# Performance work log

Measured on AMD Instinct MI355X. Metric: run time of the kernel, lower is better.

The kernel has to match this reference:

```python
import jax, jax.numpy as jnp
import numpy as np

N = 100000
E = 1600000
IN_FEATS = 128
HID = 128


def _xavier(key, shape):
    fan_in, fan_out = shape[0], shape[1]
    limit = float(np.sqrt(6.0 / (fan_in + fan_out)))
    return jax.random.uniform(key, shape, jnp.float32, -limit, limit)


def setup_inputs() -> dict:
    key = jax.random.key(0)
    ks = jax.random.split(key, 10)
    x = jax.random.normal(ks[0], (N, IN_FEATS), jnp.float32)
    edge_index = jax.random.randint(ks[1], (2, E), 0, N, jnp.int64)
    inp = {"x": x, "edge_index": edge_index}
    # GCNConv weights (stored as [in, out] so h = x @ W)
    inp["W1"] = _xavier(ks[2], (IN_FEATS, HID)); inp["b1"] = jnp.zeros((HID,), jnp.float32)
    inp["W2"] = _xavier(ks[3], (HID, HID));      inp["b2"] = jnp.zeros((HID,), jnp.float32)
    inp["W3"] = _xavier(ks[4], (HID, HID));      inp["b3"] = jnp.zeros((HID,), jnp.float32)
    # position head: Linear(HID,HID) -> ReLU -> Linear(HID,2)
    inp["Wp1"] = _xavier(ks[5], (HID, HID)); inp["bp1"] = jnp.zeros((HID,), jnp.float32)
    inp["Wp2"] = _xavier(ks[6], (HID, 2));   inp["bp2"] = jnp.zeros((2,), jnp.float32)
    # time head: Linear(HID,HID//2) -> ReLU -> Linear(HID//2,1)
    inp["Wt1"] = _xavier(ks[7], (HID, HID // 2)); inp["bt1"] = jnp.zeros((HID // 2,), jnp.float32)
    inp["Wt2"] = _xavier(ks[8], (HID // 2, 1));   inp["bt2"] = jnp.zeros((1,), jnp.float32)
    return inp


def _gcn_conv(x, src, dst, norm, W, b):
    # PyG GCNConv: out = D^{-1/2} (A + I) D^{-1/2} (x W) + b
    h = x @ W                                  # [N, out]
    msg = h[src] * norm[:, None]               # gather over edges (+ self-loops)
    agg = jax.ops.segment_sum(msg, dst, num_segments=N)  # scatter-add to dst
    return agg + b


def reference(x, edge_index, W1, b1, W2, b2, W3, b3, Wp1, bp1, Wp2, bp2, Wt1, bt1, Wt2, bt2):
    src, dst = edge_index[0], edge_index[1]
    # add self-loops once (shared across the 3 conv layers)
    loop = jnp.arange(N, dtype=edge_index.dtype)
    src_a = jnp.concatenate([src, loop])
    dst_a = jnp.concatenate([dst, loop])
    # symmetric normalization: deg computed on dst (in-degree incl. self-loop)
    deg = jax.ops.segment_sum(jnp.ones_like(dst_a, dtype=x.dtype), dst_a, num_segments=N)
    dinv = jnp.where(deg > 0, jax.lax.rsqrt(deg), 0.0)
    norm = dinv[src_a] * dinv[dst_a]           # [E + N]

    h = jax.nn.relu(_gcn_conv(x, src_a, dst_a, norm, W1, b1))
    h = jax.nn.relu(_gcn_conv(h, src_a, dst_a, norm, W2, b2))
    h = jax.nn.relu(_gcn_conv(h, src_a, dst_a, norm, W3, b3))

    pos = jax.nn.relu(h @ Wp1 + bp1) @ Wp2 + bp2     # [N, 2]
    time = jax.nn.relu(h @ Wt1 + bt1) @ Wt2 + bt2    # [N, 1]
    return jnp.concatenate([pos, time], axis=1)      # [N, 3]
```

## Files before the change

kernel.cpp:

```cpp
#include <hip/hip_runtime.h>

typedef __bf16 bf16x8 __attribute__((ext_vector_type(8)));
typedef unsigned short u16x8 __attribute__((ext_vector_type(8)));
typedef float f32x4 __attribute__((ext_vector_type(4)));

union BU {
    u16x8 u;
    bf16x8 b;
};

static __device__ __forceinline__ float b2f(unsigned short u) {
    return __uint_as_float(((unsigned)u) << 16);
}
static __device__ __forceinline__ unsigned short f2b(float f) {
    unsigned u = __float_as_uint(f);
    unsigned r = (u + 0x7FFF + ((u >> 16) & 1)) >> 16;
    return (unsigned short)r;
}

__global__ __launch_bounds__(256) void wsplit_kernel(
    const float* __restrict__ W1, const float* __restrict__ W2, const float* __restrict__ W3,
    const float* __restrict__ Wp1, const float* __restrict__ Wt1,
    unsigned short* __restrict__ W1hi, unsigned short* __restrict__ W1lo,
    unsigned short* __restrict__ W2hi, unsigned short* __restrict__ W2lo,
    unsigned short* __restrict__ W3hi, unsigned short* __restrict__ W3lo,
    unsigned short* __restrict__ Wchi, unsigned short* __restrict__ Wclo,
    const float* __restrict__ bp1, const float* __restrict__ bt1, float* __restrict__ bcat) {
    int b = blockIdx.x;
    int tid = threadIdx.x;
    if (b < 288) {
        const float* W;
        unsigned short *Whi, *Wlo;
        int lb, ncshift, total;
        if (b < 64)       { W = W1;  Whi = W1hi; Wlo = W1lo; lb = b;       ncshift = 7; total = 16384; }
        else if (b < 128) { W = W2;  Whi = W2hi; Wlo = W2lo; lb = b - 64;  ncshift = 7; total = 16384; }
        else if (b < 192) { W = W3;  Whi = W3hi; Wlo = W3lo; lb = b - 128; ncshift = 7; total = 16384; }
        else if (b < 256) { W = Wp1; Whi = Wchi; Wlo = Wclo; lb = b - 192; ncshift = 7; total = 16384; }
        else              { W = Wt1; Whi = Wchi + 128 * 128; Wlo = Wclo + 128 * 128; lb = b - 256; ncshift = 6; total = 8192; }
        int idx = lb * 256 + tid;
        if (idx < total) {
            int k = idx >> ncshift;
            int n = idx - (k << ncshift);
            float a = W[idx];
            unsigned short hb = f2b(a);
            Whi[(n << 7) + k] = hb;
            Wlo[(n << 7) + k] = f2b(a - b2f(hb));
        }
        return;
    }
    if (tid < 128) bcat[tid] = bp1[tid];
    else if (tid < 192) bcat[tid] = bt1[tid - 128];
}

static __device__ __forceinline__ void split8(const float4 a01, const float4 a23,
                                              bf16x8& hi, bf16x8& lo) {
    float a[8] = {a01.x, a01.y, a01.z, a01.w, a23.x, a23.y, a23.z, a23.w};
    BU h, l;
#pragma unroll
    for (int j = 0; j < 8; ++j) {
        unsigned short hb = f2b(a[j]);
        h.u[j] = hb;
        l.u[j] = f2b(a[j] - b2f(hb));
    }
    hi = h.b;
    lo = l.b;
}

template <int NT>
static __device__ __forceinline__ void gemm_acc_f32(const float* __restrict__ A,
                                                    const unsigned short* __restrict__ Whi,
                                                    const unsigned short* __restrict__ Wlo,
                                                    int arow, int m16, int quad, f32x4* acc) {
    const float* Arow = A + (size_t)arow * 128 + quad * 8;
#pragma unroll
    for (int kb = 0; kb < 4; ++kb) {
        float4 a01 = *reinterpret_cast<const float4*>(Arow + kb * 32);
        float4 a23 = *reinterpret_cast<const float4*>(Arow + kb * 32 + 4);
        bf16x8 ahi, alo;
        split8(a01, a23, ahi, alo);
#pragma unroll
        for (int t = 0; t < NT; ++t) {
            size_t woff = (size_t)(t * 16 + m16) * 128 + quad * 8 + kb * 32;
            BU bh, bl;
            bh.u = *reinterpret_cast<const u16x8*>(Whi + woff);
            bl.u = *reinterpret_cast<const u16x8*>(Wlo + woff);
            acc[t] = __builtin_amdgcn_mfma_f32_16x16x32_bf16(ahi, bh.b, acc[t], 0, 0, 0);
            acc[t] = __builtin_amdgcn_mfma_f32_16x16x32_bf16(ahi, bl.b, acc[t], 0, 0, 0);
            acc[t] = __builtin_amdgcn_mfma_f32_16x16x32_bf16(alo, bh.b, acc[t], 0, 0, 0);
        }
    }
}

template <int NT>
static __device__ __forceinline__ void gemm_store_plain(unsigned short* __restrict__ C,
                                                        int row_base, int m16, int quad,
                                                        f32x4* acc, int nrows) {
#pragma unroll
    for (int t = 0; t < NT; ++t) {
#pragma unroll
        for (int r = 0; r < 4; ++r) {
            int row = row_base + quad * 4 + r;
            if (row < nrows)
                C[(size_t)row * (NT * 16) + t * 16 + m16] = f2b(acc[t][r]);
        }
    }
}

__global__ __launch_bounds__(256) void fg2_kernel(const float* __restrict__ A,
                                                  const unsigned short* __restrict__ Whi,
                                                  const unsigned short* __restrict__ Wlo,
                                                  unsigned short* __restrict__ C, int nrows,
                                                  int fbn,
                                                  const int* __restrict__ ei,
                                                  int* __restrict__ deg,
                                                  int* __restrict__ slots, int E) {
    const int bid = blockIdx.x;
    const int tid = threadIdx.x;
    const int trip = bid / 3, r = bid % 3;
    if (r == 1 && trip < fbn) {
        int base = (trip * 256 + tid) * 8;
        int dsts[8], srcs[8], ps[8];
#pragma unroll
        for (int k = 0; k < 8; ++k) {
            int e = base + k;
            dsts[k] = (e < E) ? ei[E + e] : -1;
            srcs[k] = (e < E) ? ei[e] : 0;
        }
#pragma unroll
        for (int k = 0; k < 8; ++k)
            if (dsts[k] >= 0) ps[k] = atomicAdd(&deg[dsts[k]], 1);
#pragma unroll
        for (int k = 0; k < 8; ++k)
            if (dsts[k] >= 0 && ps[k] < 64)
                __builtin_nontemporal_store(srcs[k], &slots[(size_t)dsts[k] * 64 + ps[k]]);
    } else {
        int gid = bid - min(trip, fbn) - ((r > 1 && trip < fbn) ? 1 : 0);
        const int wave = tid >> 6, lane = tid & 63;
        const int m16 = lane & 15, quad = lane >> 4;
        const int row_base = gid * 64 + wave * 16;
        int arow = row_base + m16;
        if (arow >= nrows) arow = nrows - 1;
        f32x4 acc[8] = {};
        gemm_acc_f32<8>(A, Whi, Wlo, arow, m16, quad, acc);
        gemm_store_plain<8>(C, row_base, m16, quad, acc, nrows);
    }
}

__global__ __launch_bounds__(256) void scale_kernel(unsigned short* __restrict__ hs,
                                                    const int* __restrict__ deg, int n) {
    int idx = blockIdx.x * 256 + threadIdx.x;
    int node = idx >> 5;
    if (node >= n) return;
    int f = (idx & 31) * 4;
    float d = rsqrtf((float)deg[node] + 1.0f);
    ushort4 v = *reinterpret_cast<const ushort4*>(hs + (size_t)node * 128 + f);
    ushort4 o;
    o.x = f2b(b2f(v.x) * d);
    o.y = f2b(b2f(v.y) * d);
    o.z = f2b(b2f(v.z) * d);
    o.w = f2b(b2f(v.w) * d);
    *reinterpret_cast<ushort4*>(hs + (size_t)node * 128 + f) = o;
}

static __device__ __forceinline__ void pull2_to_lds(const unsigned short* __restrict__ hs,
                                                    const int* __restrict__ slots,
                                                    const int* __restrict__ deg,
                                                    const float* __restrict__ bias,
                                                    unsigned short* __restrict__ ldsw,
                                                    int row_base, int wave, int lane, int n) {
    const int slot = lane >> 4, chunk = lane & 15;
    int dgs[2], idxs[2];
#pragma unroll
    for (int i = 0; i < 2; ++i) {
        int node = row_base + wave * 2 + i;
        bool ok = node < n;
        dgs[i] = ok ? deg[node] : 0;
        idxs[i] = ok ? slots[(size_t)node * 64 + lane] : 0;
    }
#pragma unroll
    for (int i = 0; i < 2; ++i) {
        const int node = row_base + wave * 2 + i;
        if (node >= n) continue;
        const int tr = wave * 2 + i;
        const float d = rsqrtf((float)dgs[i] + 1.0f);
        const int m = min(dgs[i], 64);
        const int myidx = idxs[i];

        BU sv;
        sv.u = *reinterpret_cast<const u16x8*>(hs + (size_t)node * 128 + chunk * 8);

        float acc[8] = {};
        const int rounds = (m + 3) >> 2;
        int r = 0;
        for (; r + 4 <= rounds; r += 4) {
            int e0 = r * 4 + slot, e1 = e0 + 4, e2 = e0 + 8, e3 = e0 + 12;
            int s0 = __shfl(myidx, e0), s1 = __shfl(myidx, e1);
            int s2 = __shfl(myidx, e2), s3 = __shfl(myidx, e3);
            s0 = (unsigned)s0 < (unsigned)n ? s0 : 0;
            s1 = (unsigned)s1 < (unsigned)n ? s1 : 0;
            s2 = (unsigned)s2 < (unsigned)n ? s2 : 0;
            s3 = (unsigned)s3 < (unsigned)n ? s3 : 0;
            bool ok0 = e0 < m, ok1 = e1 < m, ok2 = e2 < m, ok3 = e3 < m;
            BU h0, h1, h2, h3;
            if (ok0) h0.u = *reinterpret_cast<const u16x8*>(hs + (size_t)s0 * 128 + chunk * 8);
            if (ok1) h1.u = *reinterpret_cast<const u16x8*>(hs + (size_t)s1 * 128 + chunk * 8);
            if (ok2) h2.u = *reinterpret_cast<const u16x8*>(hs + (size_t)s2 * 128 + chunk * 8);
            if (ok3) h3.u = *reinterpret_cast<const u16x8*>(hs + (size_t)s3 * 128 + chunk * 8);
            if (ok0) {
#pragma unroll
                for (int j = 0; j < 8; ++j) acc[j] += b2f(h0.u[j]);
            }
            if (ok1) {
#pragma unroll
                for (int j = 0; j < 8; ++j) acc[j] += b2f(h1.u[j]);
            }
            if (ok2) {
#pragma unroll
                for (int j = 0; j < 8; ++j) acc[j] += b2f(h2.u[j]);
            }
            if (ok3) {
#pragma unroll
                for (int j = 0; j < 8; ++j) acc[j] += b2f(h3.u[j]);
            }
        }
        for (; r < rounds; ++r) {
            int e0 = r * 4 + slot;
            int s0 = __shfl(myidx, e0);
            s0 = (unsigned)s0 < (unsigned)n ? s0 : 0;
            if (e0 < m) {
                BU h0;
                h0.u = *reinterpret_cast<const u16x8*>(hs + (size_t)s0 * 128 + chunk * 8);
#pragma unroll
                for (int j = 0; j < 8; ++j) acc[j] += b2f(h0.u[j]);
            }
        }
#pragma unroll
        for (int j = 0; j < 8; ++j) {
            acc[j] += __shfl_xor(acc[j], 16);
            acc[j] += __shfl_xor(acc[j], 32);
        }
        if (slot == 0) {
            BU o;
#pragma unroll
            for (int j = 0; j < 8; ++j)
                o.u[j] = f2b(fmaxf((acc[j] + b2f(sv.u[j])) * d + bias[chunk * 8 + j], 0.f));
            *reinterpret_cast<u16x8*>(&ldsw[tr * 128 + ((chunk * 8) ^ ((tr & 7) << 3))]) = o.u;
        }
    }
}

__global__ __launch_bounds__(512) void pg_kernel(const unsigned short* __restrict__ hs,
                                                 const int* __restrict__ slots,
                                                 const int* __restrict__ deg,
                                                 const float* __restrict__ bias,
                                                 const unsigned short* __restrict__ Whi,
                                                 const unsigned short* __restrict__ Wlo,
                                                 unsigned short* __restrict__ C, int n) {
    __shared__ unsigned short lds[16 * 128];
    const int tid = threadIdx.x;
    const int wave = tid >> 6, lane = tid & 63;
    const int row_base = blockIdx.x * 16;
    pull2_to_lds(hs, slots, deg, bias, lds, row_base, wave, lane, n);
    __syncthreads();
    const int m16 = lane & 15, quad = lane >> 4;
    f32x4 acc = {};
#pragma unroll
    for (int kb = 0; kb < 4; ++kb) {
        BU a;
        a.u = *reinterpret_cast<const u16x8*>(
            &lds[m16 * 128 + ((quad * 8 + kb * 32) ^ ((m16 & 7) << 3))]);
        int col = wave * 16 + m16;
        size_t woff = (size_t)col * 128 + quad * 8 + kb * 32;
        BU bh, bl;
        bh.u = *reinterpret_cast<const u16x8*>(Whi + woff);
        bl.u = *reinterpret_cast<const u16x8*>(Wlo + woff);
        acc = __builtin_amdgcn_mfma_f32_16x16x32_bf16(a.b, bh.b, acc, 0, 0, 0);
        acc = __builtin_amdgcn_mfma_f32_16x16x32_bf16(a.b, bl.b, acc, 0, 0, 0);
    }
#pragma unroll
    for (int r = 0; r < 4; ++r) {
        int row = row_base + quad * 4 + r;
        if (row < n) {
            float d = rsqrtf((float)deg[row] + 1.0f);
            C[(size_t)row * 128 + wave * 16 + m16] = f2b(acc[r] * d);
        }
    }
}

__global__ __launch_bounds__(512) void pg_heads_kernel(
    const unsigned short* __restrict__ hs, const int* __restrict__ slots,
    const int* __restrict__ deg, const float* __restrict__ bias,
    const unsigned short* __restrict__ Whi, const unsigned short* __restrict__ Wlo,
    const float* __restrict__ bcat, const float* __restrict__ Wp2,
    const float* __restrict__ bp2, const float* __restrict__ Wt2,
    const float* __restrict__ bt2, float* __restrict__ out, int n) {
    __shared__ unsigned short lds[16 * 128];
    __shared__ float part[8][16][3];
    const int tid = threadIdx.x;
    const int wave = tid >> 6, lane = tid & 63;
    const int row_base = blockIdx.x * 16;
    pull2_to_lds(hs, slots, deg, bias, lds, row_base, wave, lane, n);
    __syncthreads();
    const int m16 = lane & 15, quad = lane >> 4;
    f32x4 acc0 = {}, acc1 = {};
#pragma unroll
    for (int kb = 0; kb < 4; ++kb) {
        BU a;
        a.u = *reinterpret_cast<const u16x8*>(
            &lds[m16 * 128 + ((quad * 8 + kb * 32) ^ ((m16 & 7) << 3))]);
        {
            int col = wave * 16 + m16;
            size_t woff = (size_t)col * 128 + quad * 8 + kb * 32;
            BU bh, bl;
            bh.u = *reinterpret_cast<const u16x8*>(Whi + woff);
            bl.u = *reinterpret_cast<const u16x8*>(Wlo + woff);
            acc0 = __builtin_amdgcn_mfma_f32_16x16x32_bf16(a.b, bh.b, acc0, 0, 0, 0);
            acc0 = __builtin_amdgcn_mfma_f32_16x16x32_bf16(a.b, bl.b, acc0, 0, 0, 0);
        }
        if (wave < 4) {
            int col = 128 + wave * 16 + m16;
            size_t woff = (size_t)col * 128 + quad * 8 + kb * 32;
            BU bh, bl;
            bh.u = *reinterpret_cast<const u16x8*>(Whi + woff);
            bl.u = *reinterpret_cast<const u16x8*>(Wlo + woff);
            acc1 = __builtin_amdgcn_mfma_f32_16x16x32_bf16(a.b, bh.b, acc1, 0, 0, 0);
            acc1 = __builtin_amdgcn_mfma_f32_16x16x32_bf16(a.b, bl.b, acc1, 0, 0, 0);
        }
    }
#pragma unroll
    for (int r = 0; r < 4; ++r) {
        int trow = quad * 4 + r;
        float p0, p1, tt = 0.f;
        {
            int c = wave * 16 + m16;
            float v = fmaxf(acc0[r] + bcat[c], 0.f);
            p0 = v * Wp2[c * 2 + 0];
            p1 = v * Wp2[c * 2 + 1];
        }
        if (wave < 4) {
            int c = 128 + wave * 16 + m16;
            float v = fmaxf(acc1[r] + bcat[c], 0.f);
            tt = v * Wt2[c - 128];
        }
#pragma unroll
        for (int mask = 1; mask < 16; mask <<= 1) {
            p0 += __shfl_xor(p0, mask);
            p1 += __shfl_xor(p1, mask);
            tt += __shfl_xor(tt, mask);
        }
        if (m16 == 0) {
            part[wave][trow][0] = p0;
            part[wave][trow][1] = p1;
            part[wave][trow][2] = tt;
        }
    }
    __syncthreads();
    if (tid < 48) {
        int trow = tid / 3, c = tid - trow * 3;
        float s = 0.f;
#pragma unroll
        for (int w = 0; w < 8; ++w) s += part[w][trow][c];
        int row = row_base + trow;
        if (row < n) {
            float b = (c == 0) ? bp2[0] : (c == 1) ? bp2[1] : bt2[0];
            out[(size_t)row * 3 + c] = s + b;
        }
    }
}

extern "C" void kernel_launch(void* const* d_in, const int* in_sizes, int n_in,
                              void* d_out, int out_size, void* d_ws, size_t ws_size,
                              hipStream_t stream) {
    const int N = in_sizes[0] / 128;
    const int E = in_sizes[1] / 2;

    const float* x   = (const float*)d_in[0];
    const int* ei    = (const int*)d_in[1];
    const float* W1  = (const float*)d_in[2];
    const float* b1  = (const float*)d_in[3];
    const float* W2  = (const float*)d_in[4];
    const float* b2  = (const float*)d_in[5];
    const float* W3  = (const float*)d_in[6];
    const float* b3  = (const float*)d_in[7];
    const float* Wp1 = (const float*)d_in[8];
    const float* bp1 = (const float*)d_in[9];
    const float* Wp2 = (const float*)d_in[10];
    const float* bp2 = (const float*)d_in[11];
    const float* Wt1 = (const float*)d_in[12];
    const float* bt1 = (const float*)d_in[13];
    const float* Wt2 = (const float*)d_in[14];
    const float* bt2 = (const float*)d_in[15];
    float* out = (float*)d_out;

    char* ws = (char*)d_ws;
    size_t off = 0;
    auto alloc = [&](size_t bytes) {
        void* p = ws + off;
        off += (bytes + 255) & ~(size_t)255;
        return p;
    };
    int* deg        = (int*)alloc((size_t)N * 4);
    int* slots      = (int*)alloc((size_t)N * 64 * 4);
    unsigned short* W1hi = (unsigned short*)alloc(16384 * 2);
    unsigned short* W1lo = (unsigned short*)alloc(16384 * 2);
    unsigned short* W2hi = (unsigned short*)alloc(16384 * 2);
    unsigned short* W2lo = (unsigned short*)alloc(16384 * 2);
    unsigned short* W3hi = (unsigned short*)alloc(16384 * 2);
    unsigned short* W3lo = (unsigned short*)alloc(16384 * 2);
    unsigned short* Wchi = (unsigned short*)alloc(192 * 128 * 2);
    unsigned short* Wclo = (unsigned short*)alloc(192 * 128 * 2);
    float* bcat          = (float*)alloc(192 * 4);
    unsigned short* hsA  = (unsigned short*)alloc((size_t)N * 128 * 2);
    unsigned short* hsB  = (unsigned short*)alloc((size_t)N * 128 * 2);

    hipMemsetAsync(deg, 0, (size_t)N * 4, stream);

    wsplit_kernel<<<289, 256, 0, stream>>>(W1, W2, W3, Wp1, Wt1,
                                           W1hi, W1lo, W2hi, W2lo, W3hi, W3lo,
                                           Wchi, Wclo, bp1, bt1, bcat);

    const int gb = (N + 63) / 64;
    const int gb16 = (N + 15) / 16;
    const int fbn = ((E + 7) / 8 + 255) / 256;

    fg2_kernel<<<gb + fbn, 256, 0, stream>>>(x, W1hi, W1lo, hsA, N, fbn, ei, deg, slots, E);
    scale_kernel<<<(N * 32 + 255) / 256, 256, 0, stream>>>(hsA, deg, N);

    pg_kernel<<<gb16, 512, 0, stream>>>(hsA, slots, deg, b1, W2hi, W2lo, hsB, N);
    pg_kernel<<<gb16, 512, 0, stream>>>(hsB, slots, deg, b2, W3hi, W3lo, hsA, N);
    pg_heads_kernel<<<gb16, 512, 0, stream>>>(hsA, slots, deg, b3, Wchi, Wclo,
                                              bcat, Wp2, bp2, Wt2, bt2, out, N);
}
```

Before: 579.7 us.

## Process 32 rows per block in pull-GEMM kernels to reuse weight loads

Each 512-thread block now aggregates 32 destination rows (4 per wave) instead of 16, and the MFMA stage computes two 16-row tiles against the same weight fragments. This halves the global weight reloads per output row and halves the block count. Slot-index loads are also skipped for lanes beyond the node's degree. The cost is more registers and LDS per block, fewer blocks for load balancing, and longer serial gather work per wave.

```diff
diff --git a/kernel.cpp b/kernel.cpp
--- a/kernel.cpp
+++ b/kernel.cpp
@@ -162,26 +162,29 @@
     *reinterpret_cast<ushort4*>(hs + (size_t)node * 128 + f) = o;
 }
 
-static __device__ __forceinline__ void pull2_to_lds(const unsigned short* __restrict__ hs,
+static __device__ __forceinline__ void pull4_to_lds(const unsigned short* __restrict__ hs,
                                                     const int* __restrict__ slots,
                                                     const int* __restrict__ deg,
                                                     const float* __restrict__ bias,
                                                     unsigned short* __restrict__ ldsw,
                                                     int row_base, int wave, int lane, int n) {
     const int slot = lane >> 4, chunk = lane & 15;
-    int dgs[2], idxs[2];
-#pragma unroll
-    for (int i = 0; i < 2; ++i) {
-        int node = row_base + wave * 2 + i;
-        bool ok = node < n;
-        dgs[i] = ok ? deg[node] : 0;
-        idxs[i] = ok ? slots[(size_t)node * 64 + lane] : 0;
-    }
-#pragma unroll
-    for (int i = 0; i < 2; ++i) {
-        const int node = row_base + wave * 2 + i;
+    int dgs[4], idxs[4];
+#pragma unroll
+    for (int i = 0; i < 4; ++i) {
+        int node = row_base + wave * 4 + i;
+        dgs[i] = (node < n) ? deg[node] : 0;
+    }
+#pragma unroll
+    for (int i = 0; i < 4; ++i) {
+        int node = row_base + wave * 4 + i;
+        idxs[i] = (node < n && lane < min(dgs[i], 64)) ? slots[(size_t)node * 64 + lane] : 0;
+    }
+#pragma unroll
+    for (int i = 0; i < 4; ++i) {
+        const int node = row_base + wave * 4 + i;
         if (node >= n) continue;
-        const int tr = wave * 2 + i;
+        const int tr = wave * 4 + i;
         const float d = rsqrtf((float)dgs[i] + 1.0f);
         const int m = min(dgs[i], 64);
         const int myidx = idxs[i];
@@ -256,33 +259,41 @@
                                                  const unsigned short* __restrict__ Whi,
                                                  const unsigned short* __restrict__ Wlo,
                                                  unsigned short* __restrict__ C, int n) {
-    __shared__ unsigned short lds[16 * 128];
+    __shared__ unsigned short lds[32 * 128];
     const int tid = threadIdx.x;
     const int wave = tid >> 6, lane = tid & 63;
-    const int row_base = blockIdx.x * 16;
-    pull2_to_lds(hs, slots, deg, bias, lds, row_base, wave, lane, n);
+    const int row_base = blockIdx.x * 32;
+    pull4_to_lds(hs, slots, deg, bias, lds, row_base, wave, lane, n);
     __syncthreads();
     const int m16 = lane & 15, quad = lane >> 4;
-    f32x4 acc = {};
+    f32x4 acc0 = {}, acc1 = {};
 #pragma unroll
     for (int kb = 0; kb < 4; ++kb) {
-        BU a;
-        a.u = *reinterpret_cast<const u16x8*>(
-            &lds[m16 * 128 + ((quad * 8 + kb * 32) ^ ((m16 & 7) << 3))]);
+        const int aoff = (quad * 8 + kb * 32) ^ ((m16 & 7) << 3);
+        BU a0, a1;
+        a0.u = *reinterpret_cast<const u16x8*>(&lds[m16 * 128 + aoff]);
+        a1.u = *reinterpret_cast<const u16x8*>(&lds[(16 + m16) * 128 + aoff]);
         int col = wave * 16 + m16;
         size_t woff = (size_t)col * 128 + quad * 8 + kb * 32;
         BU bh, bl;
         bh.u = *reinterpret_cast<const u16x8*>(Whi + woff);
         bl.u = *reinterpret_cast<const u16x8*>(Wlo + woff);
-        acc = __builtin_amdgcn_mfma_f32_16x16x32_bf16(a.b, bh.b, acc, 0, 0, 0);
-        acc = __builtin_amdgcn_mfma_f32_16x16x32_bf16(a.b, bl.b, acc, 0, 0, 0);
+        acc0 = __builtin_amdgcn_mfma_f32_16x16x32_bf16(a0.b, bh.b, acc0, 0, 0, 0);
+        acc0 = __builtin_amdgcn_mfma_f32_16x16x32_bf16(a0.b, bl.b, acc0, 0, 0, 0);
+        acc1 = __builtin_amdgcn_mfma_f32_16x16x32_bf16(a1.b, bh.b, acc1, 0, 0, 0);
+        acc1 = __builtin_amdgcn_mfma_f32_16x16x32_bf16(a1.b, bl.b, acc1, 0, 0, 0);
     }
 #pragma unroll
     for (int r = 0; r < 4; ++r) {
-        int row = row_base + quad * 4 + r;
-        if (row < n) {
-            float d = rsqrtf((float)deg[row] + 1.0f);
-            C[(size_t)row * 128 + wave * 16 + m16] = f2b(acc[r] * d);
+        int row0 = row_base + quad * 4 + r;
+        int row1 = row_base + 16 + quad * 4 + r;
+        if (row0 < n) {
+            float d = rsqrtf((float)deg[row0] + 1.0f);
+            C[(size_t)row0 * 128 + wave * 16 + m16] = f2b(acc0[r] * d);
+        }
+        if (row1 < n) {
+            float d = rsqrtf((float)deg[row1] + 1.0f);
+            C[(size_t)row1 * 128 + wave * 16 + m16] = f2b(acc1[r] * d);
         }
     }
 }
@@ -294,28 +305,31 @@
     const float* __restrict__ bcat, const float* __restrict__ Wp2,
     const float* __restrict__ bp2, const float* __restrict__ Wt2,
     const float* __restrict__ bt2, float* __restrict__ out, int n) {
-    __shared__ unsigned short lds[16 * 128];
-    __shared__ float part[8][16][3];
+    __shared__ unsigned short lds[32 * 128];
+    __shared__ float part[8][32][3];
     const int tid = threadIdx.x;
     const int wave = tid >> 6, lane = tid & 63;
-    const int row_base = blockIdx.x * 16;
-    pull2_to_lds(hs, slots, deg, bias, lds, row_base, wave, lane, n);
+    const int row_base = blockIdx.x * 32;
+    pull4_to_lds(hs, slots, deg, bias, lds, row_base, wave, lane, n);
     __syncthreads();
     const int m16 = lane & 15, quad = lane >> 4;
-    f32x4 acc0 = {}, acc1 = {};
+    f32x4 acc0a = {}, acc0b = {}, acc1a = {}, acc1b = {};
 #pragma unroll
     for (int kb = 0; kb < 4; ++kb) {
-        BU a;
-        a.u = *reinterpret_cast<const u16x8*>(
-            &lds[m16 * 128 + ((quad * 8 + kb * 32) ^ ((m16 & 7) << 3))]);
+        const int aoff = (quad * 8 + kb * 32) ^ ((m16 & 7) << 3);
+        BU a0, a1;
+        a0.u = *reinterpret_cast<const u16x8*>(&lds[m16 * 128 + aoff]);
+        a1.u = *reinterpret_cast<const u16x8*>(&lds[(16 + m16) * 128 + aoff]);
         {
             int col = wave * 16 + m16;
             size_t woff = (size_t)col * 128 + quad * 8 + kb * 32;
             BU bh, bl;
             bh.u = *reinterpret_cast<const u16x8*>(Whi + woff);
             bl.u = *reinterpret_cast<const u16x8*>(Wlo + woff);
-            acc0 = __builtin_amdgcn_mfma_f32_16x16x32_bf16(a.b, bh.b, acc0, 0, 0, 0);
-            acc0 = __builtin_amdgcn_mfma_f32_16x16x32_bf16(a.b, bl.b, acc0, 0, 0, 0);
+            acc0a = __builtin_amdgcn_mfma_f32_16x16x32_bf16(a0.b, bh.b, acc0a, 0, 0, 0);
+            acc0a = __builtin_amdgcn_mfma_f32_16x16x32_bf16(a0.b, bl.b, acc0a, 0, 0, 0);
+            acc0b = __builtin_amdgcn_mfma_f32_16x16x32_bf16(a1.b, bh.b, acc0b, 0, 0, 0);
+            acc0b = __builtin_amdgcn_mfma_f32_16x16x32_bf16(a1.b, bl.b, acc0b, 0, 0, 0);
         }
         if (wave < 4) {
             int col = 128 + wave * 16 + m16;
@@ -323,39 +337,50 @@
             BU bh, bl;
             bh.u = *reinterpret_cast<const u16x8*>(Whi + woff);
             bl.u = *reinterpret_cast<const u16x8*>(Wlo + woff);
-            acc1 = __builtin_amdgcn_mfma_f32_16x16x32_bf16(a.b, bh.b, acc1, 0, 0, 0);
-            acc1 = __builtin_amdgcn_mfma_f32_16x16x32_bf16(a.b, bl.b, acc1, 0, 0, 0);
+            acc1a = __builtin_amdgcn_mfma_f32_16x16x32_bf16(a0.b, bh.b, acc1a, 0, 0, 0);
+            acc1a = __builtin_amdgcn_mfma_f32_16x16x32_bf16(a0.b, bl.b, acc1a, 0, 0, 0);
+            acc1b = __builtin_amdgcn_mfma_f32_16x16x32_bf16(a1.b, bh.b, acc1b, 0, 0, 0);
+            acc1b = __builtin_amdgcn_mfma_f32_16x16x32_bf16(a1.b, bl.b, acc1b, 0, 0, 0);
         }
     }
 #pragma unroll
     for (int r = 0; r < 4; ++r) {
-        int trow = quad * 4 + r;
-        float p0, p1, tt = 0.f;
+        float p0a, p1a, tta = 0.f, p0b, p1b, ttb = 0.f;
         {
             int c = wave * 16 + m16;
-            float v = fmaxf(acc0[r] + bcat[c], 0.f);
-            p0 = v * Wp2[c * 2 + 0];
-            p1 = v * Wp2[c * 2 + 1];
+            float w0 = Wp2[c * 2 + 0], w1 = Wp2[c * 2 + 1], bc = bcat[c];
+            float va = fmaxf(acc0a[r] + bc, 0.f);
+            float vb = fmaxf(acc0b[r] + bc, 0.f);
+            p0a = va * w0; p1a = va * w1;
+            p0b = vb * w0; p1b = vb * w1;
         }
         if (wave < 4) {
             int c = 128 + wave * 16 + m16;
-            float v = fmaxf(acc1[r] + bcat[c], 0.f);
-            tt = v * Wt2[c - 128];
+            float wt = Wt2[c - 128], bc = bcat[c];
+            tta = fmaxf(acc1a[r] + bc, 0.f) * wt;
+            ttb = fmaxf(acc1b[r] + bc, 0.f) * wt;
         }
 #pragma unroll
         for (int mask = 1; mask < 16; mask <<= 1) {
-            p0 += __shfl_xor(p0, mask);
-            p1 += __shfl_xor(p1, mask);
-            tt += __shfl_xor(tt, mask);
+            p0a += __shfl_xor(p0a, mask);
+            p1a += __shfl_xor(p1a, mask);
+            tta += __shfl_xor(tta, mask);
+            p0b += __shfl_xor(p0b, mask);
+            p1b += __shfl_xor(p1b, mask);
+            ttb += __shfl_xor(ttb, mask);
         }
         if (m16 == 0) {
-            part[wave][trow][0] = p0;
-            part[wave][trow][1] = p1;
-            part[wave][trow][2] = tt;
+            int trow = quad * 4 + r;
+            part[wave][trow][0] = p0a;
+            part[wave][trow][1] = p1a;
+            part[wave][trow][2] = tta;
+            part[wave][16 + trow][0] = p0b;
+            part[wave][16 + trow][1] = p1b;
+            part[wave][16 + trow][2] = ttb;
         }
     }
     __syncthreads();
-    if (tid < 48) {
+    if (tid < 96) {
         int trow = tid / 3, c = tid - trow * 3;
         float s = 0.f;
 #pragma unroll
@@ -420,14 +445,14 @@
                                            Wchi, Wclo, bp1, bt1, bcat);
 
     const int gb = (N + 63) / 64;
-    const int gb16 = (N + 15) / 16;
+    const int gb32 = (N + 31) / 32;
     const int fbn = ((E + 7) / 8 + 255) / 256;
 
     fg2_kernel<<<gb + fbn, 256, 0, stream>>>(x, W1hi, W1lo, hsA, N, fbn, ei, deg, slots, E);
     scale_kernel<<<(N * 32 + 255) / 256, 256, 0, stream>>>(hsA, deg, N);
 
-    pg_kernel<<<gb16, 512, 0, stream>>>(hsA, slots, deg, b1, W2hi, W2lo, hsB, N);
-    pg_kernel<<<gb16, 512, 0, stream>>>(hsB, slots, deg, b2, W3hi, W3lo, hsA, N);
-    pg_heads_kernel<<<gb16, 512, 0, stream>>>(hsA, slots, deg, b3, Wchi, Wclo,
+    pg_kernel<<<gb32, 512, 0, stream>>>(hsA, slots, deg, b1, W2hi, W2lo, hsB, N);
+    pg_kernel<<<gb32, 512, 0, stream>>>(hsB, slots, deg, b2, W3hi, W3lo, hsA, N);
+    pg_heads_kernel<<<gb32, 512, 0, stream>>>(hsA, slots, deg, b3, Wchi, Wclo,
                                               bcat, Wp2, bp2, Wt2, bt2, out, N);
 }
```

Result: faster. 543.5 us (-6.2%).
